# Performance work log

Measured on AMD Instinct MI355X. Metric: run time of the kernel, lower is better.

The kernel has to match this reference:

```python
import jax, jax.numpy as jnp
import numpy as np

DIM = 1024
HEADS = 16
HEAD_DIM = DIM // HEADS
MLP_DIM = 4 * DIM
EPS = 1e-5


def _layernorm(x, w, b):
    mu = jnp.mean(x, axis=-1, keepdims=True)
    var = jnp.mean(jnp.square(x - mu), axis=-1, keepdims=True)
    return (x - mu) * jax.lax.rsqrt(var + EPS) * w + b


def setup_inputs() -> dict:
    key = jax.random.key(0)
    ks = jax.random.split(key, 8)
    s = 0.02
    return {
        "x": jax.random.normal(ks[0], (4, 2048, DIM), dtype=jnp.float32),
        "ln1_w": jnp.ones((DIM,), jnp.float32),
        "ln1_b": jnp.zeros((DIM,), jnp.float32),
        # weights stored (in, out) so y = x @ W + b (equiv. to torch Linear W^T)
        "qkv_w": jax.random.normal(ks[1], (DIM, 3 * DIM), jnp.float32) * s,
        "qkv_b": jnp.zeros((3 * DIM,), jnp.float32),
        "proj_w": jax.random.normal(ks[2], (DIM, DIM), jnp.float32) * s,
        "proj_b": jnp.zeros((DIM,), jnp.float32),
        "ln2_w": jnp.ones((DIM,), jnp.float32),
        "ln2_b": jnp.zeros((DIM,), jnp.float32),
        "fc1_w": jax.random.normal(ks[3], (DIM, MLP_DIM), jnp.float32) * s,
        "fc1_b": jnp.zeros((MLP_DIM,), jnp.float32),
        "fc2_w": jax.random.normal(ks[4], (MLP_DIM, DIM), jnp.float32) * s,
        "fc2_b": jnp.zeros((DIM,), jnp.float32),
    }


def _attention(x, qkv_w, qkv_b, proj_w, proj_b):
    b, s, c = x.shape
    qkv = (x @ qkv_w + qkv_b).reshape(b, s, 3, HEADS, HEAD_DIM)
    q, k, v = qkv[:, :, 0], qkv[:, :, 1], qkv[:, :, 2]  # [b, s, n, d]
    scale = HEAD_DIM ** -0.5
    # naive full-score attention: [b, n, s, s]
    attn = jnp.einsum('bqnd,bknd->bnqk', q, k) * scale
    causal_mask = jnp.triu(jnp.ones((s, s), dtype=bool), k=1)
    attn = jnp.where(causal_mask, -jnp.inf, attn)
    attn = jax.nn.softmax(attn, axis=-1)
    out = jnp.einsum('bnqk,bknd->bqnd', attn, v).reshape(b, s, c)
    return out @ proj_w + proj_b


def reference(x, ln1_w, ln1_b, qkv_w, qkv_b, proj_w, proj_b,
              ln2_w, ln2_b, fc1_w, fc1_b, fc2_w, fc2_b):
    # pre-norm block (post_norm=False)
    x = x + _attention(_layernorm(x, ln1_w, ln1_b), qkv_w, qkv_b, proj_w, proj_b)
    h = _layernorm(x, ln2_w, ln2_b)
    h = jax.nn.gelu(h @ fc1_w + fc1_b, approximate=False)  # torch nn.GELU default (erf)
    x = x + (h @ fc2_w + fc2_b)
    return x
```

## Files before the change

kernel.cpp:

```cpp
#include <hip/hip_runtime.h>

#define DIM 1024
#define SEQ 2048
#define BATCH 4
#define NH 16
#define HD 64
#define MLP 4096
#define ROWS (BATCH*SEQ)

typedef __bf16 bf16x8 __attribute__((ext_vector_type(8)));
typedef float f32x4 __attribute__((ext_vector_type(4)));
typedef __attribute__((address_space(3))) void as3void;
typedef const __attribute__((address_space(1))) void as1void;

__device__ __forceinline__ unsigned short f2bf(float f) {
  unsigned u = __builtin_bit_cast(unsigned, f);
  u = (u + 0x7FFFu + ((u >> 16) & 1u)) >> 16;
  return (unsigned short)u;
}

__device__ __forceinline__ void gload_lds16(const void* gp, const void* lp) {
  __builtin_amdgcn_global_load_lds(
      (as1void*)(unsigned long long)(size_t)gp,
      (as3void*)(unsigned int)(size_t)lp,
      16, 0, 0);
}

__global__ __launch_bounds__(256) void transpose_w_kernel(
    const float* __restrict__ in, unsigned short* __restrict__ out, int K, int N)
{
  __shared__ float tile[64][65];
  const int k0 = blockIdx.y * 64, n0 = blockIdx.x * 64;
  const int tc = threadIdx.x & 63, tr = threadIdx.x >> 6;
#pragma unroll
  for (int i = 0; i < 64; i += 4)
    tile[tr + i][tc] = in[(size_t)(k0 + tr + i) * N + n0 + tc];
  __syncthreads();
#pragma unroll
  for (int i = 0; i < 64; i += 4)
    out[(size_t)(n0 + tr + i) * K + k0 + tc] = f2bf(tile[tc][tr + i]);
}

__global__ __launch_bounds__(256) void ln_kernel(
    const float* __restrict__ x, const float* __restrict__ w, const float* __restrict__ b,
    unsigned short* __restrict__ out)
{
  const int row = blockIdx.x;
  const int t = threadIdx.x;
  const int lane = t & 63, wave = t >> 6;
  const float* xr = x + (size_t)row * DIM;
  float4 v = *(const float4*)&xr[t * 4];
  float s = v.x + v.y + v.z + v.w;
  float s2 = v.x * v.x + v.y * v.y + v.z * v.z + v.w * v.w;
#pragma unroll
  for (int o = 1; o < 64; o <<= 1) {
    s += __shfl_xor(s, o);
    s2 += __shfl_xor(s2, o);
  }
  __shared__ float red[8];
  if (lane == 0) { red[wave] = s; red[4 + wave] = s2; }
  __syncthreads();
  s = red[0] + red[1] + red[2] + red[3];
  s2 = red[4] + red[5] + red[6] + red[7];
  const float mu = s * (1.f / DIM);
  const float var = s2 * (1.f / DIM) - mu * mu;
  const float rstd = rsqrtf(var + 1e-5f);
  float4 wv = *(const float4*)&w[t * 4];
  float4 bv = *(const float4*)&b[t * 4];
  ushort4 o;
  o.x = f2bf((v.x - mu) * rstd * wv.x + bv.x);
  o.y = f2bf((v.y - mu) * rstd * wv.y + bv.y);
  o.z = f2bf((v.z - mu) * rstd * wv.z + bv.z);
  o.w = f2bf((v.w - mu) * rstd * wv.w + bv.w);
  *(ushort4*)&out[(size_t)row * DIM + t * 4] = o;
}

template <int MODE>
__global__ __launch_bounds__(256) void gemm_bt(
    const unsigned short* __restrict__ A,
    const unsigned short* __restrict__ Bt,
    const float* __restrict__ bias,
    const float* resf, float* outf, unsigned short* outb,
    unsigned short* Qo, unsigned short* Ko, unsigned short* Vto,
    int M, int N, int K)
{
  __shared__ __align__(16) unsigned short sA[128 * 32];
  __shared__ __align__(16) unsigned short sB[128 * 32];
  const int tid = threadIdx.x;
  const int wave = tid >> 6, lane = tid & 63;

  const int nbx = gridDim.x;
  const int nwg = nbx * gridDim.y;
  const int bid = blockIdx.y * nbx + blockIdx.x;
  const int cpx = nwg >> 3;
  const int swz = (bid & 7) * cpx + (bid >> 3);
  const int n0 = (swz % nbx) * 128;
  const int m0 = (swz / nbx) * 128;

  const int srow = wave * 16 + (lane >> 2);
  const int scol = (lane & 3) * 8;
  const unsigned short* gA = A + (size_t)(m0 + srow) * K + scol;
  const unsigned short* gB = Bt + (size_t)(n0 + srow) * K + scol;
  unsigned short* lA0 = sA + wave * 512;
  unsigned short* lA1 = sA + 2048 + wave * 512;
  unsigned short* lB0 = sB + wave * 512;
  unsigned short* lB1 = sB + 2048 + wave * 512;
  const size_t rstep = (size_t)64 * K;

  const int wr = wave >> 1, wc = wave & 1;
  const int fl = lane & 15, fh = lane >> 4;
  f32x4 acc[4][4] = {};

  for (int k0 = 0; k0 < K; k0 += 32) {
    gload_lds16(gA + k0, lA0);
    gload_lds16(gA + rstep + k0, lA1);
    gload_lds16(gB + k0, lB0);
    gload_lds16(gB + rstep + k0, lB1);
    __syncthreads();
    bf16x8 af[4], bfr[4];
#pragma unroll
    for (int f = 0; f < 4; ++f)
      af[f] = *(const bf16x8*)&sA[(wr * 64 + f * 16 + fl) * 32 + fh * 8];
#pragma unroll
    for (int f = 0; f < 4; ++f)
      bfr[f] = *(const bf16x8*)&sB[(wc * 64 + f * 16 + fl) * 32 + fh * 8];
#pragma unroll
    for (int i = 0; i < 4; ++i)
#pragma unroll
      for (int j = 0; j < 4; ++j)
        acc[i][j] = __builtin_amdgcn_mfma_f32_16x16x32_bf16(af[i], bfr[j], acc[i][j], 0, 0, 0);
    __syncthreads();
  }

#pragma unroll
  for (int i = 0; i < 4; ++i) {
    const int rowb = m0 + wr * 64 + i * 16 + fh * 4;
#pragma unroll
    for (int j = 0; j < 4; ++j) {
      const int col = n0 + wc * 64 + j * 16 + fl;
      const float bv = bias[col];
#pragma unroll
      for (int r = 0; r < 4; ++r) {
        const int row = rowb + r;
        float v = acc[i][j][r] + bv;
        if constexpr (MODE == 0) {
          const int which = col >> 10;
          const int h = (col >> 6) & 15;
          const int d = col & 63;
          const int b = row >> 11, s = row & 2047;
          const size_t bh = (size_t)(b * 16 + h);
          if (which == 0)      Qo[(bh * SEQ + s) * HD + d] = f2bf(v * 0.125f);
          else if (which == 1) Ko[(bh * SEQ + s) * HD + d] = f2bf(v);
          else                 Vto[(bh * HD + d) * SEQ + s] = f2bf(v);
        } else if constexpr (MODE == 2) {
          const float g = 0.5f * v * (1.0f + erff(v * 0.70710678118f));
          outb[(size_t)row * N + col] = f2bf(g);
        } else {
          outf[(size_t)row * N + col] = resf[(size_t)row * N + col] + v;
        }
      }
    }
  }
}

__global__ __launch_bounds__(256, 4) void attn_kernel(
    const unsigned short* __restrict__ Q,
    const unsigned short* __restrict__ Kt,
    const unsigned short* __restrict__ Vt,
    unsigned short* __restrict__ Ao)
{
  __shared__ __align__(16) char sK[2][8192];
  __shared__ __align__(16) char sV[2][8192];
  __shared__ __align__(16) char sP[4][2048];

  const int bh = blockIdx.y;
  const int wave = threadIdx.x >> 6, lane = threadIdx.x & 63;
  const int fl = lane & 15, fh = lane >> 4;
  const char* Kb = (const char*)(Kt + (size_t)bh * SEQ * HD);
  const char* Vb = (const char*)(Vt + (size_t)bh * HD * SEQ);
  const unsigned short* Qb = Q + (size_t)bh * SEQ * HD;
  char* pbase = sP[wave];
  const int pswz = (fl & 7) << 4;
  const int b = bh >> 4, h = bh & 15;

  const int sg_row_in = lane >> 3;
  const int sg_colb = ((lane & 7) * 16) ^ (sg_row_in << 4);

  for (int phase = 0; phase < 2; ++phase) {
    const int qt = (phase == 0) ? (int)blockIdx.x : 31 - (int)blockIdx.x;
    const int qw = qt * 64 + wave * 16;
    const int nkt = qt + 1;

    bf16x8 bq[2];
#pragma unroll
    for (int kk = 0; kk < 2; ++kk)
      bq[kk] = *(const bf16x8*)&Qb[(size_t)(qw + fl) * HD + kk * 32 + fh * 8];

    f32x4 accO[4] = {};
    float mr = -1e30f, lr = 0.f;

#pragma unroll
    for (int i = 0; i < 2; ++i) {
      const int chunk = i * 4 + wave;
      const int row = chunk * 8 + sg_row_in;
      gload_lds16(Kb + (size_t)row * 128 + sg_colb, sK[0] + chunk * 1024);
      gload_lds16(Vb + (size_t)row * (SEQ * 2) + sg_colb, sV[0] + chunk * 1024);
    }
    __syncthreads();

    for (int t = 0; t < nkt; ++t) {
      const int kbase = t * 64;
      const int cur = t & 1;
      if (t + 1 < nkt) {
        const int kb2 = kbase + 64;
#pragma unroll
        for (int i = 0; i < 2; ++i) {
          const int chunk = i * 4 + wave;
          const int row = chunk * 8 + sg_row_in;
          gload_lds16(Kb + (size_t)(kb2 + row) * 128 + sg_colb, sK[cur ^ 1] + chunk * 1024);
          gload_lds16(Vb + (size_t)row * (SEQ * 2) + kb2 * 2 + sg_colb, sV[cur ^ 1] + chunk * 1024);
        }
      }

      f32x4 accT[4] = {};
      __builtin_amdgcn_s_setprio(1);
#pragma unroll
      for (int kk = 0; kk < 2; ++kk) {
        const int cb = (kk * 64 + fh * 16) ^ pswz;
#pragma unroll
        for (int fc = 0; fc < 4; ++fc) {
          const bf16x8 ak = *(const bf16x8*)(sK[cur] + (fc * 16 + fl) * 128 + cb);
          accT[fc] = __builtin_amdgcn_mfma_f32_16x16x32_bf16(ak, bq[kk], accT[fc], 0, 0, 0);
        }
      }
      __builtin_amdgcn_s_setprio(0);

      if (t == nkt - 1) {
        const int rowq = qw + fl;
#pragma unroll
        for (int fc = 0; fc < 4; ++fc)
#pragma unroll
          for (int r = 0; r < 4; ++r) {
            const int colk = kbase + fc * 16 + fh * 4 + r;
            if (colk > rowq) accT[fc][r] = -1e30f;
          }
      }

      float mx = fmaxf(fmaxf(fmaxf(accT[0][0], accT[0][1]), fmaxf(accT[0][2], accT[0][3])),
                       fmaxf(fmaxf(accT[1][0], accT[1][1]), fmaxf(accT[1][2], accT[1][3])));
      mx = fmaxf(mx, fmaxf(fmaxf(fmaxf(accT[2][0], accT[2][1]), fmaxf(accT[2][2], accT[2][3])),
                           fmaxf(fmaxf(accT[3][0], accT[3][1]), fmaxf(accT[3][2], accT[3][3]))));
      mx = fmaxf(mx, __shfl_xor(mx, 16));
      mx = fmaxf(mx, __shfl_xor(mx, 32));
      const float mnew = fmaxf(mr, mx);
      const float alpha = __expf(mr - mnew);
      mr = mnew;
      float rs = 0.f;
#pragma unroll
      for (int fc = 0; fc < 4; ++fc)
#pragma unroll
        for (int r = 0; r < 4; ++r) {
          const float p = __expf(accT[fc][r] - mnew);
          accT[fc][r] = p;
          rs += p;
        }
      rs += __shfl_xor(rs, 16);
      rs += __shfl_xor(rs, 32);
      lr = lr * alpha + rs;
#pragma unroll
      for (int dc = 0; dc < 4; ++dc)
        accO[dc] *= alpha;

#pragma unroll
      for (int fc = 0; fc < 4; ++fc) {
        uint2 pk;
        pk.x = (unsigned)f2bf(accT[fc][0]) | ((unsigned)f2bf(accT[fc][1]) << 16);
        pk.y = (unsigned)f2bf(accT[fc][2]) | ((unsigned)f2bf(accT[fc][3]) << 16);
        *(uint2*)(pbase + fl * 128 + ((fc * 32 + fh * 8) ^ pswz)) = pk;
      }

      __builtin_amdgcn_s_setprio(1);
#pragma unroll
      for (int kk = 0; kk < 2; ++kk) {
        const int cb = (kk * 64 + fh * 16) ^ pswz;
        const bf16x8 pb = *(const bf16x8*)(pbase + fl * 128 + cb);
#pragma unroll
        for (int dc = 0; dc < 4; ++dc) {
          const bf16x8 av = *(const bf16x8*)(sV[cur] + (dc * 16 + fl) * 128 + cb);
          accO[dc] = __builtin_amdgcn_mfma_f32_16x16x32_bf16(av, pb, accO[dc], 0, 0, 0);
        }
      }
      __builtin_amdgcn_s_setprio(0);

      __syncthreads();
    }

    const float inv = 1.0f / lr;
    unsigned short* orow = Ao + ((size_t)b * SEQ + qw + fl) * DIM + h * HD;
#pragma unroll
    for (int dc = 0; dc < 4; ++dc) {
      ushort4 o;
      o.x = f2bf(accO[dc][0] * inv);
      o.y = f2bf(accO[dc][1] * inv);
      o.z = f2bf(accO[dc][2] * inv);
      o.w = f2bf(accO[dc][3] * inv);
      *(ushort4*)&orow[dc * 16 + fh * 4] = o;
    }
  }
}

extern "C" void kernel_launch(void* const* d_in, const int* in_sizes, int n_in,
                              void* d_out, int out_size, void* d_ws, size_t ws_size,
                              hipStream_t stream)
{
  const float* x      = (const float*)d_in[0];
  const float* ln1_w  = (const float*)d_in[1];
  const float* ln1_b  = (const float*)d_in[2];
  const float* qkv_w  = (const float*)d_in[3];
  const float* qkv_b  = (const float*)d_in[4];
  const float* proj_w = (const float*)d_in[5];
  const float* proj_b = (const float*)d_in[6];
  const float* ln2_w  = (const float*)d_in[7];
  const float* ln2_b  = (const float*)d_in[8];
  const float* fc1_w  = (const float*)d_in[9];
  const float* fc1_b  = (const float*)d_in[10];
  const float* fc2_w  = (const float*)d_in[11];
  const float* fc2_b  = (const float*)d_in[12];
  float* out = (float*)d_out;
  unsigned short* ws = (unsigned short*)d_ws;

  unsigned short* wqkv = ws;
  unsigned short* wproj = ws + 3145728;
  unsigned short* wfc1 = ws + 4194304;
  unsigned short* wfc2 = ws + 8388608;
  unsigned short* xn1  = ws + 12582912;
  unsigned short* Qb   = ws + 20971520;
  unsigned short* Kb   = ws + 29360128;
  unsigned short* Vtb  = ws + 37748736;
  unsigned short* aout = xn1;
  unsigned short* hn   = Qb;
  unsigned short* hbuf = Kb;

  transpose_w_kernel<<<dim3(48, 16), 256, 0, stream>>>(qkv_w, wqkv, 1024, 3072);
  transpose_w_kernel<<<dim3(16, 16), 256, 0, stream>>>(proj_w, wproj, 1024, 1024);
  transpose_w_kernel<<<dim3(64, 16), 256, 0, stream>>>(fc1_w, wfc1, 1024, 4096);
  transpose_w_kernel<<<dim3(16, 64), 256, 0, stream>>>(fc2_w, wfc2, 4096, 1024);

  ln_kernel<<<ROWS, 256, 0, stream>>>(x, ln1_w, ln1_b, xn1);

  gemm_bt<0><<<dim3(24, 64), 256, 0, stream>>>(xn1, wqkv, qkv_b,
      nullptr, nullptr, nullptr, Qb, Kb, Vtb, ROWS, 3072, 1024);

  attn_kernel<<<dim3(16, 64), 256, 0, stream>>>(Qb, Kb, Vtb, aout);

  gemm_bt<1><<<dim3(8, 64), 256, 0, stream>>>(aout, wproj, proj_b,
      x, out, nullptr, nullptr, nullptr, nullptr, ROWS, 1024, 1024);

  ln_kernel<<<ROWS, 256, 0, stream>>>(out, ln2_w, ln2_b, hn);

  gemm_bt<2><<<dim3(32, 64), 256, 0, stream>>>(hn, wfc1, fc1_b,
      nullptr, nullptr, hbuf, nullptr, nullptr, nullptr, ROWS, 4096, 1024);

  gemm_bt<3><<<dim3(8, 64), 256, 0, stream>>>(hbuf, wfc2, fc2_b,
      out, out, nullptr, nullptr, nullptr, nullptr, ROWS, 1024, 4096);
}
```

Before: 598.3 us.

## Double-buffer GEMM LDS tiles with BK=64, XOR swizzle, and MFMA priority

Reworks the bf16 GEMM main loop to use two LDS buffers with a K-tile of 64. The next tile is prefetched through global_load_lds while MFMAs run on the current one, which removes one barrier per iteration and overlaps loads with compute. The load source columns are XOR-swizzled so the direct-to-LDS writes land in a bank-conflict-reduced layout that the fragment reads undo. s_setprio is raised around the MFMA block. LDS use grows to 64KB per block, which may lower occupancy.

```diff
diff --git a/kernel.cpp b/kernel.cpp
--- a/kernel.cpp
+++ b/kernel.cpp
@@ -84,8 +84,8 @@
     unsigned short* Qo, unsigned short* Ko, unsigned short* Vto,
     int M, int N, int K)
 {
-  __shared__ __align__(16) unsigned short sA[128 * 32];
-  __shared__ __align__(16) unsigned short sB[128 * 32];
+  __shared__ __align__(16) unsigned short sA[2][128 * 64];
+  __shared__ __align__(16) unsigned short sB[2][128 * 64];
   const int tid = threadIdx.x;
   const int wave = tid >> 6, lane = tid & 63;
 
@@ -97,38 +97,52 @@
   const int n0 = (swz % nbx) * 128;
   const int m0 = (swz / nbx) * 128;
 
-  const int srow = wave * 16 + (lane >> 2);
-  const int scol = (lane & 3) * 8;
-  const unsigned short* gA = A + (size_t)(m0 + srow) * K + scol;
-  const unsigned short* gB = Bt + (size_t)(n0 + srow) * K + scol;
-  unsigned short* lA0 = sA + wave * 512;
-  unsigned short* lA1 = sA + 2048 + wave * 512;
-  unsigned short* lB0 = sB + wave * 512;
-  unsigned short* lB1 = sB + 2048 + wave * 512;
-  const size_t rstep = (size_t)64 * K;
+  const int srow = tid >> 3;
+  const int sgl = (tid & 7) ^ (srow & 7);
+  const unsigned short* pA = A + (size_t)(m0 + srow) * K + sgl * 8;
+  const unsigned short* pB = Bt + (size_t)(n0 + srow) * K + sgl * 8;
 
   const int wr = wave >> 1, wc = wave & 1;
   const int fl = lane & 15, fh = lane >> 4;
   f32x4 acc[4][4] = {};
 
-  for (int k0 = 0; k0 < K; k0 += 32) {
-    gload_lds16(gA + k0, lA0);
-    gload_lds16(gA + rstep + k0, lA1);
-    gload_lds16(gB + k0, lB0);
-    gload_lds16(gB + rstep + k0, lB1);
-    __syncthreads();
-    bf16x8 af[4], bfr[4];
-#pragma unroll
-    for (int f = 0; f < 4; ++f)
-      af[f] = *(const bf16x8*)&sA[(wr * 64 + f * 16 + fl) * 32 + fh * 8];
-#pragma unroll
-    for (int f = 0; f < 4; ++f)
-      bfr[f] = *(const bf16x8*)&sB[(wc * 64 + f * 16 + fl) * 32 + fh * 8];
-#pragma unroll
-    for (int i = 0; i < 4; ++i)
-#pragma unroll
-      for (int j = 0; j < 4; ++j)
-        acc[i][j] = __builtin_amdgcn_mfma_f32_16x16x32_bf16(af[i], bfr[j], acc[i][j], 0, 0, 0);
+  const int NT = K >> 6;
+
+#pragma unroll
+  for (int j = 0; j < 4; ++j) {
+    gload_lds16(pA + (size_t)j * 32 * K, &sA[0][j * 2048 + tid * 8]);
+    gload_lds16(pB + (size_t)j * 32 * K, &sB[0][j * 2048 + tid * 8]);
+  }
+  __syncthreads();
+
+  for (int t = 0; t < NT; ++t) {
+    const int cur = t & 1;
+    if (t + 1 < NT) {
+      const size_t ko = (size_t)(t + 1) * 64;
+#pragma unroll
+      for (int j = 0; j < 4; ++j) {
+        gload_lds16(pA + (size_t)j * 32 * K + ko, &sA[cur ^ 1][j * 2048 + tid * 8]);
+        gload_lds16(pB + (size_t)j * 32 * K + ko, &sB[cur ^ 1][j * 2048 + tid * 8]);
+      }
+    }
+#pragma unroll
+    for (int ks = 0; ks < 2; ++ks) {
+      const int pg = ((ks * 4 + fh) ^ (fl & 7)) * 8;
+      bf16x8 af[4], bfr[4];
+#pragma unroll
+      for (int f = 0; f < 4; ++f)
+        af[f] = *(const bf16x8*)&sA[cur][(wr * 64 + f * 16 + fl) * 64 + pg];
+#pragma unroll
+      for (int f = 0; f < 4; ++f)
+        bfr[f] = *(const bf16x8*)&sB[cur][(wc * 64 + f * 16 + fl) * 64 + pg];
+      __builtin_amdgcn_s_setprio(1);
+#pragma unroll
+      for (int i = 0; i < 4; ++i)
+#pragma unroll
+        for (int j = 0; j < 4; ++j)
+          acc[i][j] = __builtin_amdgcn_mfma_f32_16x16x32_bf16(af[i], bfr[j], acc[i][j], 0, 0, 0);
+      __builtin_amdgcn_s_setprio(0);
+    }
     __syncthreads();
   }
 
```

Result: faster. 566.7 us (-5.3%).
